# Performance work log

Measured on AMD Instinct MI355X. Metric: run time of the kernel, lower is better.

The kernel has to match this reference:

```python
import jax, jax.numpy as jnp
import numpy as np

B, N, S, K, D = 8, 8192, 1024, 32, 64
RADIUS = 0.2
MLP = [64, 64, 128]
C_IN = 3 + D


def _fps(pts):
    # pts: [N,3] -> [S] farthest-point indices (deterministic start at index 0,
    # matching pytorch3d.sample_farthest_points default random_start_point=False)
    def body(carry, _):
        d, last = carry
        dd = jnp.sum((pts - pts[last]) ** 2, axis=-1)
        d = jnp.minimum(d, dd)
        return (d, jnp.argmax(d)), last
    init = (jnp.full((pts.shape[0],), 1e10, pts.dtype), jnp.asarray(0))
    _, idxs = jax.lax.scan(body, init, None, length=S)
    return idxs


def _ball_query(new_xyz, xyz):
    # new_xyz [B,S,3], xyz [B,N,3] -> idx [B,S,K]
    # classic PointNet++ ball query: first K points (by index order) within radius;
    # queries with fewer than K neighbors are padded by replicating the first hit.
    sqr = jnp.sum((new_xyz[:, :, None, :] - xyz[:, None, :, :]) ** 2, axis=-1)  # [B,S,N]
    cand = jnp.where(sqr <= RADIUS ** 2,
                     jnp.arange(N, dtype=jnp.int32)[None, None, :],
                     jnp.int32(N))
    idx = -jax.lax.top_k(-cand, K)[0]  # K smallest valid indices, ascending
    first = idx[..., :1]
    return jnp.where(idx == N, first, idx)


def _gather(arr, idx):
    # arr [B,N,C], idx [B,S,K] -> [B,S,K,C]
    return jax.vmap(lambda a, i: a[i])(arr, idx)


def _forward(xyz, points, attention, w0, b0, w1, b1, w2, b2):
    x = xyz.transpose(0, 2, 1)        # [B,N,3]
    p = points.transpose(0, 2, 1)     # [B,N,D]
    a = attention.transpose(0, 2, 1)  # [B,N,1]
    fps_idx = jax.vmap(_fps)(x)                      # [B,S]
    new_xyz = jax.vmap(lambda q, i: q[i])(x, fps_idx)  # [B,S,3]
    idx = _ball_query(new_xyz, x)                    # [B,S,K]
    g_norm = _gather(x, idx) - new_xyz[:, :, None, :]   # [B,S,K,3]
    feat = jnp.concatenate([g_norm, _gather(p, idx)], axis=-1)  # [B,S,K,3+D]
    new_att = jnp.mean(_gather(a, idx), axis=-2).reshape(x.shape[0], 1, -1)  # [B,1,S]
    # shared MLP (1x1 Conv2d == per-point dense), no BN (bn=False)
    h = jax.nn.relu(jnp.einsum('bskc,oc->bsko', feat, w0) + b0)
    h = jax.nn.relu(jnp.einsum('bskc,oc->bsko', h, w1) + b1)
    h = jax.nn.relu(jnp.einsum('bskc,oc->bsko', h, w2) + b2)
    new_points = jnp.max(h, axis=2)  # max-pool over nsample -> [B,S,C_out]
    return new_xyz.transpose(0, 2, 1), new_points.transpose(0, 2, 1), new_att


def setup_inputs() -> dict:
    key = jax.random.key(0)
    ks = jax.random.split(key, 9)
    xyz = jax.random.uniform(ks[0], (B, 3, N), dtype=jnp.float32)  # unit cube
    points = jax.random.normal(ks[1], (B, D, N), dtype=jnp.float32)
    attention = jax.random.uniform(ks[2], (B, 1, N), dtype=jnp.float32)
    cin = C_IN
    w0 = jax.random.normal(ks[3], (MLP[0], cin), dtype=jnp.float32) / np.sqrt(cin)
    b0 = jnp.zeros((MLP[0],), jnp.float32)
    w1 = jax.random.normal(ks[4], (MLP[1], MLP[0]), dtype=jnp.float32) / np.sqrt(MLP[0])
    b1 = jnp.zeros((MLP[1],), jnp.float32)
    w2 = jax.random.normal(ks[5], (MLP[2], MLP[1]), dtype=jnp.float32) / np.sqrt(MLP[1])
    b2 = jnp.zeros((MLP[2],), jnp.float32)
    return {"xyz": xyz, "points": points, "attention": attention,
            "w0": w0, "b0": b0, "w1": w1, "b1": b1, "w2": w2, "b2": b2}


def reference(xyz, points, attention, w0, b0, w1, b1, w2, b2):
    return _forward(xyz, points, attention, w0, b0, w1, b1, w2, b2)
```

## Files before the change

### kernel.cpp

```cpp
#include <hip/hip_runtime.h>

#define NPTS 8192
#define NSAMP 1024
#define NBATCH 8
#define KNB 32

typedef float f32x2 __attribute__((ext_vector_type(2)));

__device__ __forceinline__ f32x2 pk_add(f32x2 a, f32x2 b) {
  f32x2 d; asm("v_pk_add_f32 %0, %1, %2" : "=v"(d) : "v"(a), "v"(b)); return d;
}
__device__ __forceinline__ f32x2 pk_mul(f32x2 a, f32x2 b) {
  f32x2 d; asm("v_pk_mul_f32 %0, %1, %2" : "=v"(d) : "v"(a), "v"(b)); return d;
}

#define DPP_MIN_ROUND(k, CTRL)                                                         \
  do {                                                                                 \
    unsigned _lo = (unsigned)(k), _hi = (unsigned)((k) >> 32);                         \
    unsigned _plo = (unsigned)__builtin_amdgcn_update_dpp((int)_lo, (int)_lo, CTRL,    \
                                                          0xF, 0xF, false);            \
    unsigned _phi = (unsigned)__builtin_amdgcn_update_dpp((int)_hi, (int)_hi, CTRL,    \
                                                          0xF, 0xF, false);            \
    unsigned long long _ok = (((unsigned long long)_phi) << 32) | _plo;                \
    if (_ok < (k)) (k) = _ok;                                                          \
  } while (0)

__device__ __forceinline__ float sqdist_rn(float px, float py, float pz,
                                           float qx, float qy, float qz) {
  float dx = px - qx, dy = py - qy, dz = pz - qz;
  return __fadd_rn(__fadd_rn(__fmul_rn(dx, dx), __fmul_rn(dy, dy)), __fmul_rn(dz, dz));
}

__global__ __launch_bounds__(512) void fps_kernel(const float* __restrict__ xyz,
                                                  float* __restrict__ out_newxyz) {
  __shared__ unsigned long long wkeys[2][8];

  const int b = blockIdx.x;
  const int tid = threadIdx.x;
  const int lane = tid & 63;
  const int wv = tid >> 6;
  const float* xb = xyz + (size_t)b * 3 * NPTS;

  f32x2 X2[8], Y2[8], Z2[8], D2[8];
#pragma unroll
  for (int j = 0; j < 8; j++) {
    int n0 = tid + (2 * j) * 512, n1 = tid + (2 * j + 1) * 512;
    X2[j].x = xb[n0];            X2[j].y = xb[n1];
    Y2[j].x = xb[NPTS + n0];     Y2[j].y = xb[NPTS + n1];
    Z2[j].x = xb[2 * NPTS + n0]; Z2[j].y = xb[2 * NPTS + n1];
    D2[j].x = 1e10f;             D2[j].y = 1e10f;
  }
  float sx = xb[0], sy = xb[NPTS], sz = xb[2 * NPTS];
  float c0x = 0.f, c0y = 0.f, c0z = 0.f, c1x = 0.f, c1y = 0.f, c1z = 0.f;

  for (int t = 0; t < NSAMP; t++) {
    if (t == tid) { c0x = sx; c0y = sy; c0z = sz; }
    if (t == tid + 512) { c1x = sx; c1y = sy; c1z = sz; }

    f32x2 nqx, nqy, nqz;
    nqx.x = -sx; nqx.y = -sx;
    nqy.x = -sy; nqy.y = -sy;
    nqz.x = -sz; nqz.y = -sz;

    float bv = -1.0f;
    int bj = 0;
#pragma unroll
    for (int j = 0; j < 8; j++) {
      f32x2 dx = pk_add(X2[j], nqx);
      f32x2 dy = pk_add(Y2[j], nqy);
      f32x2 dz = pk_add(Z2[j], nqz);
      f32x2 dd = pk_add(pk_add(pk_mul(dx, dx), pk_mul(dy, dy)), pk_mul(dz, dz));
      float m0 = fminf(D2[j].x, dd.x);
      float m1 = fminf(D2[j].y, dd.y);
      D2[j].x = m0;
      D2[j].y = m1;
      if (m0 > bv) { bv = m0; bj = 2 * j; }
      if (m1 > bv) { bv = m1; bj = 2 * j + 1; }
    }
    unsigned n = (unsigned)tid + (unsigned)bj * 512u;
    unsigned long long key =
        (((unsigned long long)(~__float_as_uint(bv))) << 32) | (unsigned long long)n;

    DPP_MIN_ROUND(key, 0x111);
    DPP_MIN_ROUND(key, 0x112);
    DPP_MIN_ROUND(key, 0x114);
    DPP_MIN_ROUND(key, 0x118);
    DPP_MIN_ROUND(key, 0x142);
    DPP_MIN_ROUND(key, 0x143);

    const int par = t & 1;
    if (lane == 63) wkeys[par][wv] = key;
    __syncthreads();

    unsigned long long k8 = wkeys[par][lane & 7];
    DPP_MIN_ROUND(k8, 0xB1);
    DPP_MIN_ROUND(k8, 0x4E);
    DPP_MIN_ROUND(k8, 0x141);
    unsigned wid = (unsigned)__builtin_amdgcn_readfirstlane((int)(unsigned)k8);

    sx = xb[wid];
    sy = xb[NPTS + wid];
    sz = xb[2 * NPTS + wid];
  }

  out_newxyz[(b * 3 + 0) * NSAMP + tid] = c0x;
  out_newxyz[(b * 3 + 1) * NSAMP + tid] = c0y;
  out_newxyz[(b * 3 + 2) * NSAMP + tid] = c0z;
  out_newxyz[(b * 3 + 0) * NSAMP + 512 + tid] = c1x;
  out_newxyz[(b * 3 + 1) * NSAMP + 512 + tid] = c1y;
  out_newxyz[(b * 3 + 2) * NSAMP + 512 + tid] = c1z;
}

__global__ __launch_bounds__(256) void ballq_kernel(const float* __restrict__ xyz,
                                                    const float* __restrict__ att,
                                                    const float* __restrict__ newxyz,
                                                    int* __restrict__ idx_out,
                                                    float* __restrict__ att_out) {
  __shared__ int rowbuf[4][KNB];
  const int wv = threadIdx.x >> 6;
  const int lane = threadIdx.x & 63;
  const int g = blockIdx.x * 4 + wv;
  const int b = g >> 10;
  const int s = g & 1023;
  const float* xb = xyz + (size_t)b * 3 * NPTS;

  float qx = newxyz[(b * 3 + 0) * NSAMP + s];
  float qy = newxyz[(b * 3 + 1) * NSAMP + s];
  float qz = newxyz[(b * 3 + 2) * NSAMP + s];

  int have = 0;
  int firstn = 0;
  for (int c = 0; c < NPTS / 64; c++) {
    int n = c * 64 + lane;
    float dd = sqdist_rn(xb[n], xb[NPTS + n], xb[2 * NPTS + n], qx, qy, qz);
    bool inb = (dd <= 0.04f);
    unsigned long long m = __ballot(inb);
    if (have == 0 && m != 0ull) firstn = c * 64 + __builtin_ctzll(m);
    int pre = __popcll(m & ((1ull << lane) - 1ull));
    if (inb && (have + pre) < KNB) rowbuf[wv][have + pre] = n;
    have += __popcll(m);
    if (have >= KNB) break;
  }
  if (have > KNB) have = KNB;
  if (lane < KNB && lane >= have) rowbuf[wv][lane] = firstn;

  float av = 0.0f;
  if (lane < KNB) {
    int myidx = rowbuf[wv][lane];
    idx_out[(size_t)g * KNB + lane] = myidx;
    av = att[(size_t)b * NPTS + myidx];
  }
#pragma unroll
  for (int m = 1; m < 64; m <<= 1) av += __shfl_xor(av, m, 64);
  if (lane == 0) att_out[g] = av * 0.03125f;
}

__global__ __launch_bounds__(256) void mlp_kernel(
    const float* __restrict__ xyz, const float* __restrict__ pts,
    const float* __restrict__ newxyz, const int* __restrict__ idx,
    const float* __restrict__ w0, const float* __restrict__ b0,
    const float* __restrict__ w1, const float* __restrict__ b1,
    const float* __restrict__ w2, const float* __restrict__ b2,
    float* __restrict__ out_np) {
  const int g = blockIdx.x;
  const int b = g >> 10;
  const int s = g & 1023;
  const int t = threadIdx.x;

  __shared__ __align__(16) float feat[67 * 32];
  __shared__ __align__(16) float h0s[64 * 36];
  __shared__ __align__(16) float h1s[64 * 36];
  __shared__ int sidx[KNB];

  if (t < KNB) sidx[t] = idx[(size_t)g * KNB + t];
  __syncthreads();

  {
    int k = t & 31, rg = t >> 5;
    int n = sidx[k];
    const float* pb = pts + (size_t)b * 64 * NPTS;
    for (int r = rg; r < 67; r += 8) {
      float v;
      if (r < 3)
        v = xyz[((size_t)b * 3 + r) * NPTS + n] - newxyz[(b * 3 + r) * NSAMP + s];
      else
        v = pb[(size_t)(r - 3) * NPTS + n];
      feat[r * 32 + k] = v;
    }
  }
  __syncthreads();

  const int kq = t & 7;
  const int og = t >> 3;

  {
    float a0[8];
    float bu = b0[2 * og], bw = b0[2 * og + 1];
    a0[0] = a0[1] = a0[2] = a0[3] = bu;
    a0[4] = a0[5] = a0[6] = a0[7] = bw;
    const float* wr0 = w0 + (2 * og) * 67;
    const float* wr1 = wr0 + 67;
    for (int c = 0; c < 67; c++) {
      float4 f = *(const float4*)&feat[c * 32 + kq * 4];
      float u = wr0[c], v = wr1[c];
      a0[0] = fmaf(u, f.x, a0[0]); a0[1] = fmaf(u, f.y, a0[1]);
      a0[2] = fmaf(u, f.z, a0[2]); a0[3] = fmaf(u, f.w, a0[3]);
      a0[4] = fmaf(v, f.x, a0[4]); a0[5] = fmaf(v, f.y, a0[5]);
      a0[6] = fmaf(v, f.z, a0[6]); a0[7] = fmaf(v, f.w, a0[7]);
    }
    float4 r0, r1;
    r0.x = fmaxf(a0[0], 0.f); r0.y = fmaxf(a0[1], 0.f);
    r0.z = fmaxf(a0[2], 0.f); r0.w = fmaxf(a0[3], 0.f);
    r1.x = fmaxf(a0[4], 0.f); r1.y = fmaxf(a0[5], 0.f);
    r1.z = fmaxf(a0[6], 0.f); r1.w = fmaxf(a0[7], 0.f);
    *(float4*)&h0s[(2 * og) * 36 + kq * 4] = r0;
    *(float4*)&h0s[(2 * og + 1) * 36 + kq * 4] = r1;
  }
  __syncthreads();

  {
    float a1[8];
    float bu = b1[2 * og], bw = b1[2 * og + 1];
    a1[0] = a1[1] = a1[2] = a1[3] = bu;
    a1[4] = a1[5] = a1[6] = a1[7] = bw;
    const float* wr0 = w1 + (2 * og) * 64;
    const float* wr1 = wr0 + 64;
    for (int c = 0; c < 64; c++) {
      float4 f = *(const float4*)&h0s[c * 36 + kq * 4];
      float u = wr0[c], v = wr1[c];
      a1[0] = fmaf(u, f.x, a1[0]); a1[1] = fmaf(u, f.y, a1[1]);
      a1[2] = fmaf(u, f.z, a1[2]); a1[3] = fmaf(u, f.w, a1[3]);
      a1[4] = fmaf(v, f.x, a1[4]); a1[5] = fmaf(v, f.y, a1[5]);
      a1[6] = fmaf(v, f.z, a1[6]); a1[7] = fmaf(v, f.w, a1[7]);
    }
    float4 r0, r1;
    r0.x = fmaxf(a1[0], 0.f); r0.y = fmaxf(a1[1], 0.f);
    r0.z = fmaxf(a1[2], 0.f); r0.w = fmaxf(a1[3], 0.f);
    r1.x = fmaxf(a1[4], 0.f); r1.y = fmaxf(a1[5], 0.f);
    r1.z = fmaxf(a1[6], 0.f); r1.w = fmaxf(a1[7], 0.f);
    *(float4*)&h1s[(2 * og) * 36 + kq * 4] = r0;
    *(float4*)&h1s[(2 * og + 1) * 36 + kq * 4] = r1;
  }
  __syncthreads();

  {
    const int kq2 = t & 3;
    const int og2 = t >> 2;
    float a2[16];
    float bu = b2[2 * og2], bw = b2[2 * og2 + 1];
#pragma unroll
    for (int i = 0; i < 8; i++) { a2[i] = bu; a2[8 + i] = bw; }
    const float* wr0 = w2 + (2 * og2) * 64;
    const float* wr1 = wr0 + 64;
    for (int c = 0; c < 64; c++) {
      float4 fA = *(const float4*)&h1s[c * 36 + kq2 * 8];
      float4 fB = *(const float4*)&h1s[c * 36 + kq2 * 8 + 4];
      float u = wr0[c], v = wr1[c];
      a2[0] = fmaf(u, fA.x, a2[0]);  a2[1] = fmaf(u, fA.y, a2[1]);
      a2[2] = fmaf(u, fA.z, a2[2]);  a2[3] = fmaf(u, fA.w, a2[3]);
      a2[4] = fmaf(u, fB.x, a2[4]);  a2[5] = fmaf(u, fB.y, a2[5]);
      a2[6] = fmaf(u, fB.z, a2[6]);  a2[7] = fmaf(u, fB.w, a2[7]);
      a2[8] = fmaf(v, fA.x, a2[8]);  a2[9] = fmaf(v, fA.y, a2[9]);
      a2[10] = fmaf(v, fA.z, a2[10]); a2[11] = fmaf(v, fA.w, a2[11]);
      a2[12] = fmaf(v, fB.x, a2[12]); a2[13] = fmaf(v, fB.y, a2[13]);
      a2[14] = fmaf(v, fB.z, a2[14]); a2[15] = fmaf(v, fB.w, a2[15]);
    }
    float m0 = a2[0], m1 = a2[8];
#pragma unroll
    for (int i = 1; i < 8; i++) { m0 = fmaxf(m0, a2[i]); m1 = fmaxf(m1, a2[8 + i]); }
    m0 = fmaxf(m0, 0.f);
    m1 = fmaxf(m1, 0.f);
    m0 = fmaxf(m0, __shfl_xor(m0, 1, 64));
    m0 = fmaxf(m0, __shfl_xor(m0, 2, 64));
    m1 = fmaxf(m1, __shfl_xor(m1, 1, 64));
    m1 = fmaxf(m1, __shfl_xor(m1, 2, 64));
    if (kq2 == 0) {
      out_np[((size_t)b * 128 + 2 * og2) * NSAMP + s] = m0;
      out_np[((size_t)b * 128 + 2 * og2 + 1) * NSAMP + s] = m1;
    }
  }
}

extern "C" void kernel_launch(void* const* d_in, const int* in_sizes, int n_in,
                              void* d_out, int out_size, void* d_ws, size_t ws_size,
                              hipStream_t stream) {
  (void)in_sizes; (void)n_in; (void)out_size; (void)ws_size;
  const float* xyz = (const float*)d_in[0];
  const float* pts = (const float*)d_in[1];
  const float* att = (const float*)d_in[2];
  const float* w0 = (const float*)d_in[3];
  const float* b0 = (const float*)d_in[4];
  const float* w1 = (const float*)d_in[5];
  const float* b1 = (const float*)d_in[6];
  const float* w2 = (const float*)d_in[7];
  const float* b2 = (const float*)d_in[8];

  float* out = (float*)d_out;
  float* out_newxyz = out;
  float* out_newpts = out + NBATCH * 3 * NSAMP;
  float* out_att = out + NBATCH * 3 * NSAMP + NBATCH * 128 * NSAMP;
  int* idx_ws = (int*)d_ws;

  fps_kernel<<<NBATCH, 512, 0, stream>>>(xyz, out_newxyz);
  ballq_kernel<<<(NBATCH * NSAMP) / 4, 256, 0, stream>>>(xyz, att, out_newxyz, idx_ws, out_att);
  mlp_kernel<<<NBATCH * NSAMP, 256, 0, stream>>>(xyz, pts, out_newxyz, idx_ws,
                                                 w0, b0, w1, b1, w2, b2, out_newpts);
}
```

Measured before the change: 1.271 ms.

## Split FPS argmax into float max then index min, stage coordinates in LDS

The FPS loop's single 64-bit key DPP min-reduction becomes two steps: a 32-bit float max reduction across the wave, then a 32-bit unsigned min over the indices of lanes that hold the maximum. Point coordinates are copied into 96KB of shared memory, so each iteration fetches the selected point from LDS instead of global memory. Chosen indices are recorded and the coordinates resolved once at the end. This shortens the serial per-iteration dependency chain, at the cost of an extra equality scan and one block per CU because of the large LDS footprint.

```diff
diff --git a/kernel.cpp b/kernel.cpp
--- a/kernel.cpp
+++ b/kernel.cpp
@@ -13,6 +13,20 @@
 __device__ __forceinline__ f32x2 pk_mul(f32x2 a, f32x2 b) {
   f32x2 d; asm("v_pk_mul_f32 %0, %1, %2" : "=v"(d) : "v"(a), "v"(b)); return d;
 }
+
+#define DPP_FMAX_ROUND(v, CTRL)                                                        \
+  do {                                                                                 \
+    int _b = __float_as_int(v);                                                        \
+    int _p = __builtin_amdgcn_update_dpp(_b, _b, CTRL, 0xF, 0xF, false);               \
+    (v) = fmaxf((v), __int_as_float(_p));                                              \
+  } while (0)
+
+#define DPP_UMIN_ROUND(v, CTRL)                                                        \
+  do {                                                                                 \
+    unsigned _p = (unsigned)__builtin_amdgcn_update_dpp((int)(v), (int)(v), CTRL,      \
+                                                        0xF, 0xF, false);              \
+    if (_p < (v)) (v) = _p;                                                            \
+  } while (0)
 
 #define DPP_MIN_ROUND(k, CTRL)                                                         \
   do {                                                                                 \
@@ -33,6 +47,7 @@
 
 __global__ __launch_bounds__(512) void fps_kernel(const float* __restrict__ xyz,
                                                   float* __restrict__ out_newxyz) {
+  __shared__ float cds[NPTS * 3];
   __shared__ unsigned long long wkeys[2][8];
 
   const int b = blockIdx.x;
@@ -49,21 +64,21 @@
     Y2[j].x = xb[NPTS + n0];     Y2[j].y = xb[NPTS + n1];
     Z2[j].x = xb[2 * NPTS + n0]; Z2[j].y = xb[2 * NPTS + n1];
     D2[j].x = 1e10f;             D2[j].y = 1e10f;
-  }
-  float sx = xb[0], sy = xb[NPTS], sz = xb[2 * NPTS];
-  float c0x = 0.f, c0y = 0.f, c0z = 0.f, c1x = 0.f, c1y = 0.f, c1z = 0.f;
+    cds[n0 * 3 + 0] = X2[j].x; cds[n0 * 3 + 1] = Y2[j].x; cds[n0 * 3 + 2] = Z2[j].x;
+    cds[n1 * 3 + 0] = X2[j].y; cds[n1 * 3 + 1] = Y2[j].y; cds[n1 * 3 + 2] = Z2[j].y;
+  }
+  __syncthreads();
+
+  float sx = cds[0], sy = cds[1], sz = cds[2];
+  unsigned c0i = 0, c1i = 0;
 
   for (int t = 0; t < NSAMP; t++) {
-    if (t == tid) { c0x = sx; c0y = sy; c0z = sz; }
-    if (t == tid + 512) { c1x = sx; c1y = sy; c1z = sz; }
-
     f32x2 nqx, nqy, nqz;
     nqx.x = -sx; nqx.y = -sx;
     nqy.x = -sy; nqy.y = -sy;
     nqz.x = -sz; nqz.y = -sz;
 
-    float bv = -1.0f;
-    int bj = 0;
+    float bvx = -1.0f, bvy = -1.0f;
 #pragma unroll
     for (int j = 0; j < 8; j++) {
       f32x2 dx = pk_add(X2[j], nqx);
@@ -74,41 +89,63 @@
       float m1 = fminf(D2[j].y, dd.y);
       D2[j].x = m0;
       D2[j].y = m1;
-      if (m0 > bv) { bv = m0; bj = 2 * j; }
-      if (m1 > bv) { bv = m1; bj = 2 * j + 1; }
-    }
-    unsigned n = (unsigned)tid + (unsigned)bj * 512u;
+      bvx = fmaxf(bvx, m0);
+      bvy = fmaxf(bvy, m1);
+    }
+    float bv = fmaxf(bvx, bvy);
+
+    DPP_FMAX_ROUND(bv, 0x111);
+    DPP_FMAX_ROUND(bv, 0x112);
+    DPP_FMAX_ROUND(bv, 0x114);
+    DPP_FMAX_ROUND(bv, 0x118);
+    DPP_FMAX_ROUND(bv, 0x142);
+    DPP_FMAX_ROUND(bv, 0x143);
+    float wval = __int_as_float(__builtin_amdgcn_readlane(__float_as_int(bv), 63));
+
+    int bj = 16;
+#pragma unroll
+    for (int j = 7; j >= 0; j--) {
+      if (D2[j].y == wval) bj = 2 * j + 1;
+      if (D2[j].x == wval) bj = 2 * j;
+    }
+    unsigned n = (unsigned)tid + ((unsigned)bj << 9);
+
+    DPP_UMIN_ROUND(n, 0x111);
+    DPP_UMIN_ROUND(n, 0x112);
+    DPP_UMIN_ROUND(n, 0x114);
+    DPP_UMIN_ROUND(n, 0x118);
+    DPP_UMIN_ROUND(n, 0x142);
+    DPP_UMIN_ROUND(n, 0x143);
+
     unsigned long long key =
-        (((unsigned long long)(~__float_as_uint(bv))) << 32) | (unsigned long long)n;
-
-    DPP_MIN_ROUND(key, 0x111);
-    DPP_MIN_ROUND(key, 0x112);
-    DPP_MIN_ROUND(key, 0x114);
-    DPP_MIN_ROUND(key, 0x118);
-    DPP_MIN_ROUND(key, 0x142);
-    DPP_MIN_ROUND(key, 0x143);
-
+        (((unsigned long long)(~__float_as_uint(wval))) << 32) | (unsigned long long)n;
     const int par = t & 1;
     if (lane == 63) wkeys[par][wv] = key;
     __syncthreads();
-
     unsigned long long k8 = wkeys[par][lane & 7];
     DPP_MIN_ROUND(k8, 0xB1);
     DPP_MIN_ROUND(k8, 0x4E);
     DPP_MIN_ROUND(k8, 0x141);
     unsigned wid = (unsigned)__builtin_amdgcn_readfirstlane((int)(unsigned)k8);
 
-    sx = xb[wid];
-    sy = xb[NPTS + wid];
-    sz = xb[2 * NPTS + wid];
-  }
-
-  out_newxyz[(b * 3 + 0) * NSAMP + tid] = c0x;
-  out_newxyz[(b * 3 + 1) * NSAMP + tid] = c0y;
-  out_newxyz[(b * 3 + 2) * NSAMP + tid] = c0z;
-  out_newxyz[(b * 3 + 0) * NSAMP + 512 + tid] = c1x;
-  out_newxyz[(b * 3 + 1) * NSAMP + 512 + tid] = c1y;
-  out_newxyz[(b * 3 + 2) * NSAMP + 512 + tid] = c1z;
+    if (t + 1 == tid) c0i = wid;
+    if (t + 1 == tid + 512) c1i = wid;
+
+    sx = cds[wid * 3 + 0];
+    sy = cds[wid * 3 + 1];
+    sz = cds[wid * 3 + 2];
+  }
+
+  {
+    float ax = cds[c0i * 3 + 0], ay = cds[c0i * 3 + 1], az = cds[c0i * 3 + 2];
+    float bx = cds[c1i * 3 + 0], by = cds[c1i * 3 + 1], bz = cds[c1i * 3 + 2];
+    out_newxyz[(b * 3 + 0) * NSAMP + tid] = ax;
+    out_newxyz[(b * 3 + 1) * NSAMP + tid] = ay;
+    out_newxyz[(b * 3 + 2) * NSAMP + tid] = az;
+    out_newxyz[(b * 3 + 0) * NSAMP + 512 + tid] = bx;
+    out_newxyz[(b * 3 + 1) * NSAMP + 512 + tid] = by;
+    out_newxyz[(b * 3 + 2) * NSAMP + 512 + tid] = bz;
+  }
 }
 
 __global__ __launch_bounds__(256) void ballq_kernel(const float* __restrict__ xyz,
```

Result: faster. 1.226 ms (-3.6%).
